# Kernel tuning notes

Measured on AMD Instinct MI355X. Metric: run time of the kernel, lower is better.

The kernel has to match this reference:

```python
import jax, jax.numpy as jnp
import numpy as np

N = 100000      # nodes
E = 1600000     # edges
F_IN = 128      # in_feat
H = 128         # hidden_dim
C = 40          # num_class


def setup_inputs() -> dict:
    key = jax.random.key(0)
    ks = jax.random.split(key, 4)
    x = jax.random.normal(ks[0], (N, F_IN), dtype=jnp.float32)
    edge_index = jax.random.randint(ks[1], (2, E), 0, N, dtype=jnp.int32)
    # glorot-ish init for the two GCN layers
    W1 = jax.random.normal(ks[2], (F_IN, H), dtype=jnp.float32) * (1.0 / np.sqrt(F_IN))
    b1 = jnp.zeros((H,), dtype=jnp.float32)
    W2 = jax.random.normal(ks[3], (H, C), dtype=jnp.float32) * (1.0 / np.sqrt(H))
    b2 = jnp.zeros((C,), dtype=jnp.float32)
    return {"x": x, "edge_index": edge_index, "W1": W1, "b1": b1, "W2": W2, "b2": b2}


def _gcn_conv(x, W, b, row, col, norm, n_nodes):
    # GCNConv: linear transform, then normalized sum-aggregation over edges, + bias
    h = x @ W                                  # [N, d_out]
    msg = h[row] * norm[:, None]               # gather sources, scale  [E', d_out]
    out = jax.ops.segment_sum(msg, col, num_segments=n_nodes)  # scatter-add to targets
    return out + b


def reference(x, edge_index, W1, b1, W2, b2):
    n_nodes = x.shape[0]
    # add self-loops (PyG GCNConv default)
    loops = jnp.arange(n_nodes, dtype=edge_index.dtype)
    row = jnp.concatenate([edge_index[0], loops])  # sources
    col = jnp.concatenate([edge_index[1], loops])  # targets
    # symmetric normalization: deg computed at targets with unit edge weights
    deg = jax.ops.segment_sum(jnp.ones_like(col, dtype=x.dtype), col, num_segments=n_nodes)
    dis = jnp.where(deg > 0, jax.lax.rsqrt(jnp.maximum(deg, 1e-12)), 0.0)
    norm = dis[row] * dis[col]                 # [E+N]

    h = jax.nn.relu(_gcn_conv(x, W1, b1, row, col, norm, n_nodes))
    out = _gcn_conv(h, W2, b2, row, col, norm, n_nodes)
    return out
```

## Files before the change

### kernel.cpp

```cpp
#include <hip/hip_runtime.h>
#include <hip/hip_bf16.h>


#define FB_SHIFT 9

__device__ __forceinline__ unsigned bf16rn(float f) {
    unsigned x = __float_as_uint(f);
    unsigned r = ((x >> 16) & 1u) + 0x7fffu;
    return (x + r) >> 16;
}
__device__ __forceinline__ float bf_lo(unsigned u) { return __uint_as_float(u << 16); }
__device__ __forceinline__ float bf_hi(unsigned u) { return __uint_as_float(u & 0xffff0000u); }

typedef __bf16 bf16x8 __attribute__((ext_vector_type(8)));
typedef float  f32x4  __attribute__((ext_vector_type(4)));

__global__ __launch_bounds__(256) void k_bcount(const int* __restrict__ col,
                                                int* __restrict__ btot, int E) {
    __shared__ int h[256];
    const int tid = threadIdx.x;
    h[tid] = 0;
    __syncthreads();
    const int base = blockIdx.x * 4096;
#pragma unroll
    for (int k = 0; k < 16; ++k) {
        int e = base + k * 256 + tid;
        if (e < E) atomicAdd(&h[col[e] >> FB_SHIFT], 1);
    }
    __syncthreads();
    int v = h[tid];
    if (v > 0) atomicAdd(&btot[tid], v);
}

__global__ __launch_bounds__(256) void k_bscan(const int* __restrict__ btot,
                                               int* __restrict__ bbase,
                                               int* __restrict__ bcur) {
    __shared__ int s[256];
    const int t = threadIdx.x;
    int v = btot[t];
    s[t] = v;
    __syncthreads();
#pragma unroll
    for (int off = 1; off < 256; off <<= 1) {
        int u = (t >= off) ? s[t - off] : 0;
        __syncthreads();
        s[t] += u;
        __syncthreads();
    }
    int excl = s[t] - v;
    bbase[t] = excl;
    bcur[t] = excl;
    if (t == 255) bbase[256] = s[255];
}

__global__ __launch_bounds__(256) void k_binfill(const int* __restrict__ row,
                                                 const int* __restrict__ col,
                                                 int* __restrict__ bcur,
                                                 unsigned* __restrict__ bins, int E) {
    __shared__ int hist[256];
    __shared__ int scn[256];
    __shared__ int gbase[256];
    __shared__ int rcnt[256];
    __shared__ unsigned stage[4096];
    __shared__ unsigned char bkts[4096];

    const int tid = threadIdx.x;
    const int base = blockIdx.x * 4096;

    hist[tid] = 0;
    rcnt[tid] = 0;
    __syncthreads();

    unsigned mypk[16];
    int      myb[16];
#pragma unroll
    for (int k = 0; k < 16; ++k) {
        int e = base + k * 256 + tid;
        if (e < E) {
            int r = row[e], c = col[e];
            int b = c >> FB_SHIFT;
            mypk[k] = ((unsigned)r << FB_SHIFT) | (unsigned)(c & ((1 << FB_SHIFT) - 1));
            myb[k] = b;
            atomicAdd(&hist[b], 1);
        } else {
            myb[k] = -1;
        }
    }
    __syncthreads();

    int v = hist[tid];
    scn[tid] = v;
    __syncthreads();
#pragma unroll
    for (int off = 1; off < 256; off <<= 1) {
        int t = (tid >= off) ? scn[tid - off] : 0;
        __syncthreads();
        scn[tid] += t;
        __syncthreads();
    }
    int excl = scn[tid] - v;
    __syncthreads();
    scn[tid] = excl;
    __syncthreads();

#pragma unroll
    for (int k = 0; k < 16; ++k) {
        int b = myb[k];
        if (b >= 0) {
            int slot = scn[b] + atomicAdd(&rcnt[b], 1);
            stage[slot] = mypk[k];
            bkts[slot] = (unsigned char)b;
        }
    }

    if (hist[tid] > 0) gbase[tid] = atomicAdd(&bcur[tid], hist[tid]);
    __syncthreads();

    int total = scn[255] + hist[255];
    for (int s = tid; s < total; s += 256) {
        unsigned u = stage[s];
        int b = bkts[s];
        bins[gbase[b] + (s - scn[b])] = u;
    }
}

__global__ __launch_bounds__(256) void k_fill2(const unsigned* __restrict__ bins,
                                               const int* __restrict__ bbase,
                                               int* __restrict__ rowptr,
                                               float* __restrict__ dis,
                                               int* __restrict__ pair, int N) {
    __shared__ int cnt[512];
    __shared__ int lcur[512];
    __shared__ int ssum[256];
    const int tid = threadIdx.x;
    const int b = blockIdx.x;
    const int n0 = b << FB_SHIFT;
    const int start = bbase[b];
    const int end = bbase[b + 1];

    cnt[tid] = 0;
    cnt[tid + 256] = 0;
    __syncthreads();

    for (int i = start + tid; i < end; i += 256)
        atomicAdd(&cnt[bins[i] & ((1 << FB_SHIFT) - 1)], 1);
    __syncthreads();

    int c0 = cnt[2 * tid], c1 = cnt[2 * tid + 1];
    int vsum = c0 + c1;
    ssum[tid] = vsum;
    __syncthreads();
#pragma unroll
    for (int off = 1; off < 256; off <<= 1) {
        int u = (tid >= off) ? ssum[tid - off] : 0;
        __syncthreads();
        ssum[tid] += u;
        __syncthreads();
    }
    int e0 = start + ssum[tid] - vsum;
    int e1 = e0 + c0;
    lcur[2 * tid] = e0;
    lcur[2 * tid + 1] = e1;
    int node0 = n0 + 2 * tid;
    int node1 = node0 + 1;
    if (node0 <= N) rowptr[node0] = e0;
    if (node1 <= N) rowptr[node1] = e1;
    if (node0 < N) dis[node0] = rsqrtf((float)(c0 + 1));
    if (node1 < N) dis[node1] = rsqrtf((float)(c1 + 1));
    __syncthreads();

    for (int i = start + tid; i < end; i += 256) {
        unsigned u = bins[i];
        int pos = atomicAdd(&lcur[u & ((1 << FB_SHIFT) - 1)], 1);
        pair[pos] = (int)(u >> FB_SHIFT);
    }
}

__global__ __launch_bounds__(256) void k_cvt(const float* __restrict__ x,
                                             const float* __restrict__ dis,
                                             unsigned* __restrict__ xb, int n64) {
    int i = blockIdx.x * 256 + threadIdx.x;
    if (i >= n64) return;
    float2 v = ((const float2*)x)[i];
    float d = dis[i >> 6];
    xb[i] = bf16rn(v.x * d) | (bf16rn(v.y * d) << 16);
}

__global__ __launch_bounds__(256) void k_cvtW(const float* __restrict__ W1,
                                              unsigned* __restrict__ Wt) {
    int t = blockIdx.x * 256 + threadIdx.x;
    if (t >= 8192) return;
    int n = t >> 6, kk = (t & 63) * 2;
    unsigned lo = bf16rn(W1[(size_t)kk * 128 + n]);
    unsigned hi = bf16rn(W1[(size_t)(kk + 1) * 128 + n]);
    Wt[t] = lo | (hi << 16);
}

__global__ __launch_bounds__(256) void k_cvtW2(const float* __restrict__ W2,
                                               unsigned* __restrict__ W2t) {
    int t = blockIdx.x * 256 + threadIdx.x;
    if (t >= 3072) return;
    int n = t >> 6, kk = (t & 63) * 2;
    unsigned lo = 0, hi = 0;
    if (n < 40) {
        lo = bf16rn(W2[(size_t)kk * 40 + n]);
        hi = bf16rn(W2[(size_t)(kk + 1) * 40 + n]);
    }
    W2t[t] = lo | (hi << 16);
}

__global__ __launch_bounds__(256) void k_gather1(const unsigned* __restrict__ xb,
                                                 const int* __restrict__ rowptr,
                                                 const int* __restrict__ pair,
                                                 const float* __restrict__ dis,
                                                 unsigned* __restrict__ xab, int N) {
    int gw = (blockIdx.x * 256 + threadIdx.x) >> 6;
    int lane = threadIdx.x & 63;
    if (gw >= N) return;
    float dv = dis[gw];
    unsigned us = xb[(size_t)gw * 64 + lane];
    float2 acc = make_float2(bf_lo(us), bf_hi(us));
    int j = rowptr[gw], je = rowptr[gw + 1];

    for (; j + 7 < je; j += 8) {
        int r0 = pair[j],     r1 = pair[j + 1], r2 = pair[j + 2], r3 = pair[j + 3];
        int r4 = pair[j + 4], r5 = pair[j + 5], r6 = pair[j + 6], r7 = pair[j + 7];
        unsigned a0 = xb[(size_t)r0 * 64 + lane];
        unsigned a1 = xb[(size_t)r1 * 64 + lane];
        unsigned a2 = xb[(size_t)r2 * 64 + lane];
        unsigned a3 = xb[(size_t)r3 * 64 + lane];
        unsigned a4 = xb[(size_t)r4 * 64 + lane];
        unsigned a5 = xb[(size_t)r5 * 64 + lane];
        unsigned a6 = xb[(size_t)r6 * 64 + lane];
        unsigned a7 = xb[(size_t)r7 * 64 + lane];
        acc.x += bf_lo(a0); acc.y += bf_hi(a0);
        acc.x += bf_lo(a1); acc.y += bf_hi(a1);
        acc.x += bf_lo(a2); acc.y += bf_hi(a2);
        acc.x += bf_lo(a3); acc.y += bf_hi(a3);
        acc.x += bf_lo(a4); acc.y += bf_hi(a4);
        acc.x += bf_lo(a5); acc.y += bf_hi(a5);
        acc.x += bf_lo(a6); acc.y += bf_hi(a6);
        acc.x += bf_lo(a7); acc.y += bf_hi(a7);
    }
    for (; j + 3 < je; j += 4) {
        int r0 = pair[j], r1 = pair[j + 1], r2 = pair[j + 2], r3 = pair[j + 3];
        unsigned a0 = xb[(size_t)r0 * 64 + lane];
        unsigned a1 = xb[(size_t)r1 * 64 + lane];
        unsigned a2 = xb[(size_t)r2 * 64 + lane];
        unsigned a3 = xb[(size_t)r3 * 64 + lane];
        acc.x += bf_lo(a0); acc.y += bf_hi(a0);
        acc.x += bf_lo(a1); acc.y += bf_hi(a1);
        acc.x += bf_lo(a2); acc.y += bf_hi(a2);
        acc.x += bf_lo(a3); acc.y += bf_hi(a3);
    }
    for (; j < je; ++j) {
        unsigned a0 = xb[(size_t)pair[j] * 64 + lane];
        acc.x += bf_lo(a0); acc.y += bf_hi(a0);
    }
    xab[(size_t)gw * 64 + lane] = bf16rn(dv * acc.x) | (bf16rn(dv * acc.y) << 16);
}

__global__ __launch_bounds__(256) void k_gemm1(const unsigned* __restrict__ Ab,
                                               const unsigned* __restrict__ Wt,
                                               const float* __restrict__ bias,
                                               unsigned* __restrict__ Hb, int M) {
    __shared__ char smem[69632];
    char* Abase = smem;
    char* Bbase = smem + 34816;

    const int tid = threadIdx.x;
    const int r0 = blockIdx.x * 128;

#pragma unroll
    for (int s = 0; s < 8; ++s) {
        int l = tid + s * 256;
        int row = l >> 4, q = l & 15;
        uint4 va = *(const uint4*)(Ab + (size_t)(r0 + row) * 64 + q * 4);
        *(uint4*)(Abase + row * 272 + q * 16) = va;
        uint4 vb = *(const uint4*)(Wt + (size_t)row * 64 + q * 4);
        *(uint4*)(Bbase + row * 272 + q * 16) = vb;
    }
    __syncthreads();

    const int wv = tid >> 6, lane = tid & 63;
    const int quad = lane >> 4, mcol = lane & 15;

    f32x4 acc[2][8];
#pragma unroll
    for (int rt = 0; rt < 2; ++rt)
#pragma unroll
        for (int ct = 0; ct < 8; ++ct) acc[rt][ct] = (f32x4){0.f, 0.f, 0.f, 0.f};

#pragma unroll
    for (int ks = 0; ks < 4; ++ks) {
        bf16x8 a[2], b[8];
#pragma unroll
        for (int rt = 0; rt < 2; ++rt) {
            int row = wv * 32 + rt * 16 + mcol;
            a[rt] = *(const bf16x8*)(Abase + row * 272 + ks * 64 + quad * 16);
        }
#pragma unroll
        for (int ct = 0; ct < 8; ++ct) {
            int n = ct * 16 + mcol;
            b[ct] = *(const bf16x8*)(Bbase + n * 272 + ks * 64 + quad * 16);
        }
#pragma unroll
        for (int rt = 0; rt < 2; ++rt)
#pragma unroll
            for (int ct = 0; ct < 8; ++ct)
                acc[rt][ct] = __builtin_amdgcn_mfma_f32_16x16x32_bf16(
                    a[rt], b[ct], acc[rt][ct], 0, 0, 0);
    }
    __syncthreads();

    unsigned short* Hs = (unsigned short*)smem;
#pragma unroll
    for (int rt = 0; rt < 2; ++rt)
#pragma unroll
        for (int ct = 0; ct < 8; ++ct) {
            float bb = bias[ct * 16 + mcol];
#pragma unroll
            for (int r = 0; r < 4; ++r) {
                float v = acc[rt][ct][r] + bb;
                v = v > 0.f ? v : 0.f;
                int orow = wv * 32 + rt * 16 + quad * 4 + r;
                Hs[orow * 136 + ct * 16 + mcol] = (unsigned short)bf16rn(v);
            }
        }
    __syncthreads();

    int row = tid >> 1, hf = tid & 1;
    if (r0 + row < M) {
        const uint4* s4 = (const uint4*)(smem + row * 272 + hf * 128);
        uint4* d4 = (uint4*)(Hb + (size_t)(r0 + row) * 64 + hf * 32);
#pragma unroll
        for (int q = 0; q < 8; ++q) d4[q] = s4[q];
    }
}

__global__ __launch_bounds__(256) void k_gemm2(const unsigned* __restrict__ Hb,
                                               const unsigned* __restrict__ W2t,
                                               const float* __restrict__ dis,
                                               unsigned* __restrict__ Zb, int M) {
    __shared__ char smem[47872];
    __shared__ float ldis[128];
    char* Abase = smem;
    char* Bbase = smem + 34816;

    const int tid = threadIdx.x;
    const int r0 = blockIdx.x * 128;

#pragma unroll
    for (int s = 0; s < 8; ++s) {
        int l = tid + s * 256;
        int row = l >> 4, q = l & 15;
        uint4 va = *(const uint4*)(Hb + (size_t)(r0 + row) * 64 + q * 4);
        *(uint4*)(Abase + row * 272 + q * 16) = va;
    }
#pragma unroll
    for (int s = 0; s < 3; ++s) {
        int l = tid + s * 256;
        int row = l >> 4, q = l & 15;
        uint4 vb = *(const uint4*)(W2t + (size_t)row * 64 + q * 4);
        *(uint4*)(Bbase + row * 272 + q * 16) = vb;
    }
    if (tid < 128) {
        int rr = r0 + tid;
        ldis[tid] = (rr < M) ? dis[rr] : 0.f;
    }
    __syncthreads();

    const int wv = tid >> 6, lane = tid & 63;
    const int quad = lane >> 4, mcol = lane & 15;

    f32x4 acc[2][3];
#pragma unroll
    for (int rt = 0; rt < 2; ++rt)
#pragma unroll
        for (int ct = 0; ct < 3; ++ct) acc[rt][ct] = (f32x4){0.f, 0.f, 0.f, 0.f};

#pragma unroll
    for (int ks = 0; ks < 4; ++ks) {
        bf16x8 a[2], b[3];
#pragma unroll
        for (int rt = 0; rt < 2; ++rt) {
            int row = wv * 32 + rt * 16 + mcol;
            a[rt] = *(const bf16x8*)(Abase + row * 272 + ks * 64 + quad * 16);
        }
#pragma unroll
        for (int ct = 0; ct < 3; ++ct) {
            int n = ct * 16 + mcol;
            b[ct] = *(const bf16x8*)(Bbase + n * 272 + ks * 64 + quad * 16);
        }
#pragma unroll
        for (int rt = 0; rt < 2; ++rt)
#pragma unroll
            for (int ct = 0; ct < 3; ++ct)
                acc[rt][ct] = __builtin_amdgcn_mfma_f32_16x16x32_bf16(
                    a[rt], b[ct], acc[rt][ct], 0, 0, 0);
    }
    __syncthreads();

    unsigned short* Hs = (unsigned short*)smem;
#pragma unroll
    for (int rt = 0; rt < 2; ++rt)
#pragma unroll
        for (int ct = 0; ct < 3; ++ct) {
#pragma unroll
            for (int r = 0; r < 4; ++r) {
                int orow = wv * 32 + rt * 16 + quad * 4 + r;
                float v = acc[rt][ct][r] * ldis[orow];
                Hs[orow * 56 + ct * 16 + mcol] = (unsigned short)bf16rn(v);
            }
        }
    __syncthreads();

    if (tid < 128) {
        int rr = r0 + tid;
        if (rr < M) {
            const uint4* s4 = (const uint4*)(smem + tid * 112);
            uint4* d4 = (uint4*)(Zb + (size_t)rr * 20);
#pragma unroll
            for (int q = 0; q < 5; ++q) d4[q] = s4[q];
        }
    }
}

__global__ __launch_bounds__(256) void k_gather2(const unsigned* __restrict__ zb,
                                                 const int* __restrict__ rowptr,
                                                 const int* __restrict__ pair,
                                                 const float* __restrict__ dis,
                                                 const float* __restrict__ b2,
                                                 float* __restrict__ out, int N) {
    int gw = (blockIdx.x * 256 + threadIdx.x) >> 6;
    int lane = threadIdx.x & 63;
    if (gw >= N) return;
    int sub = lane >> 5;
    int sl  = lane & 31;
    int f   = (sl < 20) ? sl : 19;

    float2 acc = make_float2(0.f, 0.f);
    float dv = dis[gw];
    if (sub == 0) {
        unsigned u = zb[(size_t)gw * 20 + f];
        acc.x = bf_lo(u); acc.y = bf_hi(u);
    }

    int j = rowptr[gw], je = rowptr[gw + 1];
    for (; j + 7 < je; j += 8) {
        int rA = pair[j + sub];
        int rB = pair[j + 2 + sub];
        int rC = pair[j + 4 + sub];
        int rD = pair[j + 6 + sub];
        unsigned uA = zb[(size_t)rA * 20 + f];
        unsigned uB = zb[(size_t)rB * 20 + f];
        unsigned uC = zb[(size_t)rC * 20 + f];
        unsigned uD = zb[(size_t)rD * 20 + f];
        acc.x += bf_lo(uA); acc.y += bf_hi(uA);
        acc.x += bf_lo(uB); acc.y += bf_hi(uB);
        acc.x += bf_lo(uC); acc.y += bf_hi(uC);
        acc.x += bf_lo(uD); acc.y += bf_hi(uD);
    }
    for (; j + 3 < je; j += 4) {
        int rA = pair[j + sub];
        int rB = pair[j + 2 + sub];
        unsigned uA = zb[(size_t)rA * 20 + f];
        unsigned uB = zb[(size_t)rB * 20 + f];
        acc.x += bf_lo(uA); acc.y += bf_hi(uA);
        acc.x += bf_lo(uB); acc.y += bf_hi(uB);
    }
    for (; j + 1 < je; j += 2) {
        unsigned u = zb[(size_t)pair[j + sub] * 20 + f];
        acc.x += bf_lo(u); acc.y += bf_hi(u);
    }
    if (j < je && sub == 0) {
        unsigned u = zb[(size_t)pair[j] * 20 + f];
        acc.x += bf_lo(u); acc.y += bf_hi(u);
    }

    float bx = __shfl(acc.x, sl + 32, 64);
    float by = __shfl(acc.y, sl + 32, 64);
    if (sub == 0 && sl < 20) {
        float2 bias = ((const float2*)b2)[sl];
        float2 res = make_float2((acc.x + bx) * dv + bias.x,
                                 (acc.y + by) * dv + bias.y);
        ((float2*)(out + (size_t)gw * 40))[sl] = res;
    }
}

extern "C" void kernel_launch(void* const* d_in, const int* in_sizes, int n_in,
                              void* d_out, int out_size, void* d_ws, size_t ws_size,
                              hipStream_t stream) {
    const float* x  = (const float*)d_in[0];
    const int*   ei = (const int*)d_in[1];
    const float* W1 = (const float*)d_in[2];
    const float* b1 = (const float*)d_in[3];
    const float* W2 = (const float*)d_in[4];
    const float* b2 = (const float*)d_in[5];
    float* out = (float*)d_out;

    const int N = in_sizes[0] / 128;
    const int E = in_sizes[1] / 2;
    const int* row = ei;
    const int* col = ei + E;

    const int Np = (N + 255) & ~255;
    const int nbuck = (N + (1 << FB_SHIFT) - 1) >> FB_SHIFT;

    int*      rowptr = (int*)d_ws;
    int*      btot   = rowptr + Np + 256;
    int*      bbase  = btot + 256;
    int*      bcur   = bbase + 320;
    float*    dis    = (float*)(bcur + 256);
    unsigned* Wt     = (unsigned*)(dis + Np);
    unsigned* W2t    = Wt + 8192;
    int*      pair   = (int*)(W2t + 3072);
    unsigned* xb     = (unsigned*)(pair + E);
    unsigned* xab    = xb + (size_t)N * 64;
    unsigned* hb     = xab + (size_t)N * 64;
    unsigned* zb     = hb + (size_t)N * 64;
    unsigned* bins   = (unsigned*)xab;

    hipMemsetAsync(btot, 0, 256 * sizeof(int), stream);
    k_bcount<<<(E + 4095) / 4096, 256, 0, stream>>>(col, btot, E);
    k_bscan<<<1, 256, 0, stream>>>(btot, bbase, bcur);
    k_binfill<<<(E + 4095) / 4096, 256, 0, stream>>>(row, col, bcur, bins, E);
    k_fill2<<<nbuck, 256, 0, stream>>>(bins, bbase, rowptr, dis, pair, N);

    k_cvt<<<(N * 64 + 255) / 256, 256, 0, stream>>>(x, dis, xb, N * 64);
    k_cvtW<<<32, 256, 0, stream>>>(W1, Wt);
    k_cvtW2<<<12, 256, 0, stream>>>(W2, W2t);

    k_gather1<<<(N + 3) / 4, 256, 0, stream>>>(xb, rowptr, pair, dis, xab, N);
    k_gemm1<<<(N + 127) / 128, 256, 0, stream>>>(xab, Wt, b1, hb, N);

    k_gemm2<<<(N + 127) / 128, 256, 0, stream>>>(hb, W2t, dis, zb, N);
    k_gather2<<<(N + 3) / 4, 256, 0, stream>>>(zb, rowptr, pair, dis, b2, out, N);
}
```

Measured before the change: 309.2 us.

## Fuse GEMM1 and GEMM2 via shared memory, merge conversion kernels, deepen gather2 unroll

The two dense GEMM kernels are merged into one. The ReLU'd hidden tile stays in LDS and feeds the second MFMA GEMM directly, so the bf16 hidden matrix is never written to or read back from global memory. The three conversion kernels are combined into one launch, and gather2 gains a 16-edge unrolled loop for more memory-level parallelism. The fused kernel reuses LDS regions carefully and keeps both accumulator sets live, which may raise register pressure and lower occupancy.

```diff
diff --git a/kernel.cpp b/kernel.cpp
--- a/kernel.cpp
+++ b/kernel.cpp
@@ -176,37 +176,36 @@
     }
 }
 
-__global__ __launch_bounds__(256) void k_cvt(const float* __restrict__ x,
-                                             const float* __restrict__ dis,
-                                             unsigned* __restrict__ xb, int n64) {
+__global__ __launch_bounds__(256) void k_cvtall(const float* __restrict__ x,
+                                                const float* __restrict__ dis,
+                                                unsigned* __restrict__ xb,
+                                                const float* __restrict__ W1,
+                                                const float* __restrict__ W2,
+                                                unsigned* __restrict__ Wt,
+                                                unsigned* __restrict__ W2t, int n64) {
     int i = blockIdx.x * 256 + threadIdx.x;
-    if (i >= n64) return;
-    float2 v = ((const float2*)x)[i];
-    float d = dis[i >> 6];
-    xb[i] = bf16rn(v.x * d) | (bf16rn(v.y * d) << 16);
-}
-
-__global__ __launch_bounds__(256) void k_cvtW(const float* __restrict__ W1,
-                                              unsigned* __restrict__ Wt) {
-    int t = blockIdx.x * 256 + threadIdx.x;
-    if (t >= 8192) return;
-    int n = t >> 6, kk = (t & 63) * 2;
-    unsigned lo = bf16rn(W1[(size_t)kk * 128 + n]);
-    unsigned hi = bf16rn(W1[(size_t)(kk + 1) * 128 + n]);
-    Wt[t] = lo | (hi << 16);
-}
-
-__global__ __launch_bounds__(256) void k_cvtW2(const float* __restrict__ W2,
-                                               unsigned* __restrict__ W2t) {
-    int t = blockIdx.x * 256 + threadIdx.x;
-    if (t >= 3072) return;
-    int n = t >> 6, kk = (t & 63) * 2;
-    unsigned lo = 0, hi = 0;
-    if (n < 40) {
-        lo = bf16rn(W2[(size_t)kk * 40 + n]);
-        hi = bf16rn(W2[(size_t)(kk + 1) * 40 + n]);
-    }
-    W2t[t] = lo | (hi << 16);
+    if (i < n64) {
+        float2 v = ((const float2*)x)[i];
+        float d = dis[i >> 6];
+        xb[i] = bf16rn(v.x * d) | (bf16rn(v.y * d) << 16);
+        return;
+    }
+    int t = i - n64;
+    if (t < 8192) {
+        int n = t >> 6, kk = (t & 63) * 2;
+        unsigned lo = bf16rn(W1[(size_t)kk * 128 + n]);
+        unsigned hi = bf16rn(W1[(size_t)(kk + 1) * 128 + n]);
+        Wt[t] = lo | (hi << 16);
+    } else if (t < 8192 + 3072) {
+        int u = t - 8192;
+        int n = u >> 6, kk = (u & 63) * 2;
+        unsigned lo = 0, hi = 0;
+        if (n < 40) {
+            lo = bf16rn(W2[(size_t)kk * 40 + n]);
+            hi = bf16rn(W2[(size_t)(kk + 1) * 40 + n]);
+        }
+        W2t[u] = lo | (hi << 16);
+    }
 }
 
 __global__ __launch_bounds__(256) void k_gather1(const unsigned* __restrict__ xb,
@@ -260,13 +259,16 @@
     xab[(size_t)gw * 64 + lane] = bf16rn(dv * acc.x) | (bf16rn(dv * acc.y) << 16);
 }
 
-__global__ __launch_bounds__(256) void k_gemm1(const unsigned* __restrict__ Ab,
-                                               const unsigned* __restrict__ Wt,
-                                               const float* __restrict__ bias,
-                                               unsigned* __restrict__ Hb, int M) {
-    __shared__ char smem[69632];
+__global__ __launch_bounds__(256) void k_gemm12(const unsigned* __restrict__ Ab,
+                                                const unsigned* __restrict__ Wt,
+                                                const unsigned* __restrict__ W2t,
+                                                const float* __restrict__ bias,
+                                                const float* __restrict__ dis,
+                                                unsigned* __restrict__ Zb, int M) {
+    __shared__ char smem[70144];
     char* Abase = smem;
     char* Bbase = smem + 34816;
+    float* ldis = (float*)(smem + 69632);
 
     const int tid = threadIdx.x;
     const int r0 = blockIdx.x * 128;
@@ -280,16 +282,20 @@
         uint4 vb = *(const uint4*)(Wt + (size_t)row * 64 + q * 4);
         *(uint4*)(Bbase + row * 272 + q * 16) = vb;
     }
+    if (tid < 128) {
+        int rr = r0 + tid;
+        ldis[tid] = (rr < M) ? dis[rr] : 0.f;
+    }
     __syncthreads();
 
     const int wv = tid >> 6, lane = tid & 63;
     const int quad = lane >> 4, mcol = lane & 15;
 
-    f32x4 acc[2][8];
+    f32x4 acc1[2][8];
 #pragma unroll
     for (int rt = 0; rt < 2; ++rt)
 #pragma unroll
-        for (int ct = 0; ct < 8; ++ct) acc[rt][ct] = (f32x4){0.f, 0.f, 0.f, 0.f};
+        for (int ct = 0; ct < 8; ++ct) acc1[rt][ct] = (f32x4){0.f, 0.f, 0.f, 0.f};
 
 #pragma unroll
     for (int ks = 0; ks < 4; ++ks) {
@@ -308,12 +314,12 @@
         for (int rt = 0; rt < 2; ++rt)
 #pragma unroll
             for (int ct = 0; ct < 8; ++ct)
-                acc[rt][ct] = __builtin_amdgcn_mfma_f32_16x16x32_bf16(
-                    a[rt], b[ct], acc[rt][ct], 0, 0, 0);
-    }
-    __syncthreads();
-
-    unsigned short* Hs = (unsigned short*)smem;
+                acc1[rt][ct] = __builtin_amdgcn_mfma_f32_16x16x32_bf16(
+                    a[rt], b[ct], acc1[rt][ct], 0, 0, 0);
+    }
+    __syncthreads();
+
+    unsigned short* Hs = (unsigned short*)Bbase;
 #pragma unroll
     for (int rt = 0; rt < 2; ++rt)
 #pragma unroll
@@ -321,63 +327,26 @@
             float bb = bias[ct * 16 + mcol];
 #pragma unroll
             for (int r = 0; r < 4; ++r) {
-                float v = acc[rt][ct][r] + bb;
+                float v = acc1[rt][ct][r] + bb;
                 v = v > 0.f ? v : 0.f;
                 int orow = wv * 32 + rt * 16 + quad * 4 + r;
                 Hs[orow * 136 + ct * 16 + mcol] = (unsigned short)bf16rn(v);
             }
         }
-    __syncthreads();
-
-    int row = tid >> 1, hf = tid & 1;
-    if (r0 + row < M) {
-        const uint4* s4 = (const uint4*)(smem + row * 272 + hf * 128);
-        uint4* d4 = (uint4*)(Hb + (size_t)(r0 + row) * 64 + hf * 32);
-#pragma unroll
-        for (int q = 0; q < 8; ++q) d4[q] = s4[q];
-    }
-}
-
-__global__ __launch_bounds__(256) void k_gemm2(const unsigned* __restrict__ Hb,
-                                               const unsigned* __restrict__ W2t,
-                                               const float* __restrict__ dis,
-                                               unsigned* __restrict__ Zb, int M) {
-    __shared__ char smem[47872];
-    __shared__ float ldis[128];
-    char* Abase = smem;
-    char* Bbase = smem + 34816;
-
-    const int tid = threadIdx.x;
-    const int r0 = blockIdx.x * 128;
-
-#pragma unroll
-    for (int s = 0; s < 8; ++s) {
-        int l = tid + s * 256;
-        int row = l >> 4, q = l & 15;
-        uint4 va = *(const uint4*)(Hb + (size_t)(r0 + row) * 64 + q * 4);
-        *(uint4*)(Abase + row * 272 + q * 16) = va;
-    }
 #pragma unroll
     for (int s = 0; s < 3; ++s) {
         int l = tid + s * 256;
         int row = l >> 4, q = l & 15;
         uint4 vb = *(const uint4*)(W2t + (size_t)row * 64 + q * 4);
-        *(uint4*)(Bbase + row * 272 + q * 16) = vb;
-    }
-    if (tid < 128) {
-        int rr = r0 + tid;
-        ldis[tid] = (rr < M) ? dis[rr] : 0.f;
-    }
-    __syncthreads();
-
-    const int wv = tid >> 6, lane = tid & 63;
-    const int quad = lane >> 4, mcol = lane & 15;
-
-    f32x4 acc[2][3];
+        *(uint4*)(Abase + row * 272 + q * 16) = vb;
+    }
+    __syncthreads();
+
+    f32x4 acc2[2][3];
 #pragma unroll
     for (int rt = 0; rt < 2; ++rt)
 #pragma unroll
-        for (int ct = 0; ct < 3; ++ct) acc[rt][ct] = (f32x4){0.f, 0.f, 0.f, 0.f};
+        for (int ct = 0; ct < 3; ++ct) acc2[rt][ct] = (f32x4){0.f, 0.f, 0.f, 0.f};
 
 #pragma unroll
     for (int ks = 0; ks < 4; ++ks) {
@@ -385,23 +354,23 @@
 #pragma unroll
         for (int rt = 0; rt < 2; ++rt) {
             int row = wv * 32 + rt * 16 + mcol;
-            a[rt] = *(const bf16x8*)(Abase + row * 272 + ks * 64 + quad * 16);
+            a[rt] = *(const bf16x8*)(Bbase + row * 272 + ks * 64 + quad * 16);
         }
 #pragma unroll
         for (int ct = 0; ct < 3; ++ct) {
             int n = ct * 16 + mcol;
-            b[ct] = *(const bf16x8*)(Bbase + n * 272 + ks * 64 + quad * 16);
+            b[ct] = *(const bf16x8*)(Abase + n * 272 + ks * 64 + quad * 16);
         }
 #pragma unroll
         for (int rt = 0; rt < 2; ++rt)
 #pragma unroll
             for (int ct = 0; ct < 3; ++ct)
-                acc[rt][ct] = __builtin_amdgcn_mfma_f32_16x16x32_bf16(
-                    a[rt], b[ct], acc[rt][ct], 0, 0, 0);
-    }
-    __syncthreads();
-
-    unsigned short* Hs = (unsigned short*)smem;
+                acc2[rt][ct] = __builtin_amdgcn_mfma_f32_16x16x32_bf16(
+                    a[rt], b[ct], acc2[rt][ct], 0, 0, 0);
+    }
+    __syncthreads();
+
+    unsigned short* Zs = (unsigned short*)(Abase + 16384);
 #pragma unroll
     for (int rt = 0; rt < 2; ++rt)
 #pragma unroll
@@ -409,8 +378,8 @@
 #pragma unroll
             for (int r = 0; r < 4; ++r) {
                 int orow = wv * 32 + rt * 16 + quad * 4 + r;
-                float v = acc[rt][ct][r] * ldis[orow];
-                Hs[orow * 56 + ct * 16 + mcol] = (unsigned short)bf16rn(v);
+                float v = acc2[rt][ct][r] * ldis[orow];
+                Zs[orow * 56 + ct * 16 + mcol] = (unsigned short)bf16rn(v);
             }
         }
     __syncthreads();
@@ -418,7 +387,7 @@
     if (tid < 128) {
         int rr = r0 + tid;
         if (rr < M) {
-            const uint4* s4 = (const uint4*)(smem + tid * 112);
+            const uint4* s4 = (const uint4*)(Abase + 16384 + tid * 112);
             uint4* d4 = (uint4*)(Zb + (size_t)rr * 20);
 #pragma unroll
             for (int q = 0; q < 5; ++q) d4[q] = s4[q];
@@ -447,6 +416,32 @@
     }
 
     int j = rowptr[gw], je = rowptr[gw + 1];
+    for (; j + 15 < je; j += 16) {
+        int rA = pair[j + sub];
+        int rB = pair[j + 2 + sub];
+        int rC = pair[j + 4 + sub];
+        int rD = pair[j + 6 + sub];
+        int rE = pair[j + 8 + sub];
+        int rF = pair[j + 10 + sub];
+        int rG = pair[j + 12 + sub];
+        int rH = pair[j + 14 + sub];
+        unsigned uA = zb[(size_t)rA * 20 + f];
+        unsigned uB = zb[(size_t)rB * 20 + f];
+        unsigned uC = zb[(size_t)rC * 20 + f];
+        unsigned uD = zb[(size_t)rD * 20 + f];
+        unsigned uE = zb[(size_t)rE * 20 + f];
+        unsigned uF = zb[(size_t)rF * 20 + f];
+        unsigned uG = zb[(size_t)rG * 20 + f];
+        unsigned uH = zb[(size_t)rH * 20 + f];
+        acc.x += bf_lo(uA); acc.y += bf_hi(uA);
+        acc.x += bf_lo(uB); acc.y += bf_hi(uB);
+        acc.x += bf_lo(uC); acc.y += bf_hi(uC);
+        acc.x += bf_lo(uD); acc.y += bf_hi(uD);
+        acc.x += bf_lo(uE); acc.y += bf_hi(uE);
+        acc.x += bf_lo(uF); acc.y += bf_hi(uF);
+        acc.x += bf_lo(uG); acc.y += bf_hi(uG);
+        acc.x += bf_lo(uH); acc.y += bf_hi(uH);
+    }
     for (; j + 7 < je; j += 8) {
         int rA = pair[j + sub];
         int rB = pair[j + 2 + sub];
@@ -517,8 +512,7 @@
     int*      pair   = (int*)(W2t + 3072);
     unsigned* xb     = (unsigned*)(pair + E);
     unsigned* xab    = xb + (size_t)N * 64;
-    unsigned* hb     = xab + (size_t)N * 64;
-    unsigned* zb     = hb + (size_t)N * 64;
+    unsigned* zb     = xab + (size_t)N * 64;
     unsigned* bins   = (unsigned*)xab;
 
     hipMemsetAsync(btot, 0, 256 * sizeof(int), stream);
@@ -527,13 +521,12 @@
     k_binfill<<<(E + 4095) / 4096, 256, 0, stream>>>(row, col, bcur, bins, E);
     k_fill2<<<nbuck, 256, 0, stream>>>(bins, bbase, rowptr, dis, pair, N);
 
-    k_cvt<<<(N * 64 + 255) / 256, 256, 0, stream>>>(x, dis, xb, N * 64);
-    k_cvtW<<<32, 256, 0, stream>>>(W1, Wt);
-    k_cvtW2<<<12, 256, 0, stream>>>(W2, W2t);
+    k_cvtall<<<(N * 64 + 11264 + 255) / 256, 256, 0, stream>>>(
+        x, dis, xb, W1, W2, Wt, W2t, N * 64);
 
     k_gather1<<<(N + 3) / 4, 256, 0, stream>>>(xb, rowptr, pair, dis, xab, N);
-    k_gemm1<<<(N + 127) / 128, 256, 0, stream>>>(xab, Wt, b1, hb, N);
-
-    k_gemm2<<<(N + 127) / 128, 256, 0, stream>>>(hb, W2t, dis, zb, N);
+
+    k_gemm12<<<(N + 127) / 128, 256, 0, stream>>>(xab, Wt, W2t, b1, dis, zb, N);
+
     k_gather2<<<(N + 3) / 4, 256, 0, stream>>>(zb, rowptr, pair, dis, b2, out, N);
 }
```

After: 286.0 us. 1.08x faster.
